# Optimization experiments

Measured on AMD Instinct MI355X. Metric: run time of the kernel, lower is better.

Reference implementation:

```python
import jax, jax.numpy as jnp
import numpy as np
import math

D_MODEL = 1024
N_HEADS = 16
FFN_DIM = 4096
B, L = 8, 1024
LN_EPS = 1e-5


def setup_inputs() -> dict:
    key = jax.random.key(0)
    ks = jax.random.split(key, 16)
    s = 1.0 / math.sqrt(D_MODEL)
    sf = 1.0 / math.sqrt(FFN_DIM)
    # weights stored [in, out] (transposed vs torch nn.Linear)
    return {
        "x": jax.random.normal(ks[0], (B, L, D_MODEL), dtype=jnp.float32),
        "Wq": jax.random.normal(ks[1], (D_MODEL, D_MODEL), dtype=jnp.float32) * s,
        "bq": jnp.zeros((D_MODEL,), jnp.float32),
        "Wk": jax.random.normal(ks[2], (D_MODEL, D_MODEL), dtype=jnp.float32) * s,
        "bk": jnp.zeros((D_MODEL,), jnp.float32),
        "Wv": jax.random.normal(ks[3], (D_MODEL, D_MODEL), dtype=jnp.float32) * s,
        "bv": jnp.zeros((D_MODEL,), jnp.float32),
        "Wo": jax.random.normal(ks[4], (D_MODEL, D_MODEL), dtype=jnp.float32) * s,
        "bo": jnp.zeros((D_MODEL,), jnp.float32),
        "W1": jax.random.normal(ks[5], (D_MODEL, FFN_DIM), dtype=jnp.float32) * s,
        "b1": jnp.zeros((FFN_DIM,), jnp.float32),
        "W2": jax.random.normal(ks[6], (FFN_DIM, D_MODEL), dtype=jnp.float32) * sf,
        "b2": jnp.zeros((D_MODEL,), jnp.float32),
        "gamma": jnp.ones((D_MODEL,), jnp.float32),
        "beta": jnp.zeros((D_MODEL,), jnp.float32),
    }


def reference(x, Wq, bq, Wk, bk, Wv, bv, Wo, bo, W1, b1, W2, b2, gamma, beta):
    Bb, Ll, D = x.shape
    H = N_HEADS
    E = D // H
    scale = 1.0 / math.sqrt(E)
    # multi-head attention (dropout is identity in eval)
    q = (x @ Wq + bq).reshape(Bb, Ll, H, E)
    k = (x @ Wk + bk).reshape(Bb, Ll, H, E)
    v = (x @ Wv + bv).reshape(Bb, Ll, H, E)
    scores = jnp.einsum('blhe,bshe->bhls', q, k)  # [B,H,L,L]
    A = jax.nn.softmax(scale * scores, axis=-1)
    ctx = jnp.einsum('bhls,bshd->blhd', A, v).reshape(Bb, Ll, D)
    attn_out = ctx @ Wo + bo
    x = x + attn_out
    # FFN: conv1d kernel_size=1 == pointwise linear; exact (erf) GELU as in F.gelu
    h = jax.nn.gelu(x @ W1 + b1, approximate=False)
    x = x + (h @ W2 + b2)
    # LayerNorm
    mu = jnp.mean(x, axis=-1, keepdims=True)
    var = jnp.mean(jnp.square(x - mu), axis=-1, keepdims=True)
    out = (x - mu) * jax.lax.rsqrt(var + LN_EPS) * gamma + beta
    return out
```

## Files before the change

kernel.cpp:

```cpp
#include <hip/hip_runtime.h>
#include <cmath>

typedef __attribute__((ext_vector_type(8))) _Float16 half8;
typedef __attribute__((ext_vector_type(4))) _Float16 half4;
typedef __attribute__((ext_vector_type(4))) float f32x4;

__device__ __forceinline__ void glds16(const void* g, void* l) {
  __builtin_amdgcn_global_load_lds(
      (__attribute__((address_space(1))) const void*)g,
      (__attribute__((address_space(3))) void*)l, 16, 0, 0);
}

__device__ __forceinline__ float fast_erf(float x) {
  float ax = fabsf(x);
  float t = 1.0f / (1.0f + 0.3275911f * ax);
  float y = t * (0.254829592f +
            t * (-0.284496736f +
            t * (1.421413741f +
            t * (-1.453152027f + t * 1.061405429f))));
  float r = 1.0f - y * __expf(-ax * ax);
  return copysignf(r, x);
}

__global__ __launch_bounds__(256) void k_cvt(const float* __restrict__ in,
                                             _Float16* __restrict__ out) {
  int i = (blockIdx.x * 256 + threadIdx.x) * 8;
  const f32x4* p = (const f32x4*)(in + i);
  f32x4 a = p[0], b = p[1];
  half8 h;
  h[0] = (_Float16)a[0]; h[1] = (_Float16)a[1]; h[2] = (_Float16)a[2]; h[3] = (_Float16)a[3];
  h[4] = (_Float16)b[0]; h[5] = (_Float16)b[1]; h[6] = (_Float16)b[2]; h[7] = (_Float16)b[3];
  *(half8*)(out + i) = h;
}

__global__ __launch_bounds__(256) void k_wt(const float* __restrict__ W,
                                            _Float16* __restrict__ Wt, int K, int N) {
  __shared__ float t[32][33];
  int x = threadIdx.x & 31, y4 = (threadIdx.x >> 5) << 2;
  int n0 = blockIdx.x << 5, k0 = blockIdx.y << 5;
#pragma unroll
  for (int r = 0; r < 4; ++r) t[y4 + r][x] = W[(size_t)(k0 + y4 + r) * N + n0 + x];
  __syncthreads();
#pragma unroll
  for (int r = 0; r < 4; ++r) Wt[(size_t)(n0 + y4 + r) * K + k0 + x] = (_Float16)t[x][y4 + r];
}

__global__ void k_biascat(const float* __restrict__ a, const float* __restrict__ b,
                          const float* __restrict__ c, float* __restrict__ o) {
  int i = blockIdx.x * 256 + threadIdx.x;
  const float* s = i < 1024 ? a : (i < 2048 ? b : c);
  o[i] = s[i & 1023];
}

template <int BM, int EPI>
__global__ __launch_bounds__(512, 2) void k_gemm8(
    const _Float16* __restrict__ A, const _Float16* __restrict__ Bt,
    const float* __restrict__ bias, const float* __restrict__ res,
    float* __restrict__ outf, _Float16* __restrict__ outh, int M, int N, int K) {
  constexpr int MR = BM / 32;
  constexpr int MH2 = MR / 2;
  constexpr int AL = BM * 64;
  constexpr int BL = 256 * 64;
  constexpr int ABYTES = BM * 128;
  constexpr int BBYTES = 256 * 128;
  constexpr int AB2 = 2 * ABYTES;
  __shared__ _Float16 lds[2 * (AL + BL)];
  const char* ldsc = (const char*)lds;

  const int tid = threadIdx.x;
  const int lane = tid & 63;
  const int w = tid >> 6, wr = w >> 2, wc = w & 3;
  const int l15 = lane & 15, grp = lane >> 4;

  const int gx = gridDim.x;
  const int nwg = gx * gridDim.y;
  const int lid = blockIdx.y * gx + blockIdx.x;
  const int wid = (lid & 7) * (nwg >> 3) + (lid >> 3);
  const int m0 = (wid / gx) * BM, n0 = (wid % gx) * 256;

  const int m2 = (l15 >> 2) & 1, m01 = l15 & 3;
  const int chunk0 = (m2 << 2) | (grp ^ m01);
  const int aoff0 = wr * 2048 + l15 * 128 + chunk0 * 16;
  const int aoff1 = aoff0 ^ 64;
  const int boff0 = wc * 2048 + l15 * 128 + chunk0 * 16;
  const int boff1 = boff0 ^ 64;

  const int srow = tid >> 3;
  const int scs8 = ((tid & 7) ^ (srow & 7)) * 8;
  const int NK = K >> 6;

  f32x4 acc[MR][4] = {};
  half8 af[MH2][2], bf[2][2];

#define STG_A(J, MHH, KN)                                                      \
  _Pragma("unroll") for (int s = 0; s < BM / 128; ++s)                         \
      glds16(A + (size_t)(m0 + (MHH) * (BM / 2) + s * 64 + srow) * K +         \
                 (size_t)(KN)*64 + scs8,                                       \
             lds + (J)*AL + ((MHH) * (BM / 2) + s * 64) * 64 + tid * 8);
#define STG_B(J, NHH, KN)                                                      \
  _Pragma("unroll") for (int s = 0; s < 2; ++s)                                \
      glds16(Bt + (size_t)(n0 + (NHH)*128 + s * 64 + srow) * K +               \
                  (size_t)(KN)*64 + scs8,                                      \
             lds + 2 * AL + (J)*BL + ((NHH)*128 + s * 64) * 64 + tid * 8);

#define VM_C asm volatile("s_waitcnt vmcnt(2)" ::: "memory")
#define VM_NONE

#define PHASE(J, MHQ, NHQ, RA, RB, STGSTMT, VMSTMT)                            \
  {                                                                            \
    if constexpr (RA) {                                                        \
      _Pragma("unroll") for (int i = 0; i < MH2; ++i) {                        \
        af[i][0] = *(const half8*)(ldsc + (J)*ABYTES +                         \
                                   ((MHQ)*MH2 + i) * 4096 + aoff0);            \
        af[i][1] = *(const half8*)(ldsc + (J)*ABYTES +                         \
                                   ((MHQ)*MH2 + i) * 4096 + aoff1);            \
      }                                                                        \
    }                                                                          \
    if constexpr (RB) {                                                        \
      _Pragma("unroll") for (int n = 0; n < 2; ++n) {                          \
        bf[n][0] = *(const half8*)(ldsc + AB2 + (J)*BBYTES +                   \
                                   ((NHQ)*2 + n) * 8192 + boff0);              \
        bf[n][1] = *(const half8*)(ldsc + AB2 + (J)*BBYTES +                   \
                                   ((NHQ)*2 + n) * 8192 + boff1);              \
      }                                                                        \
    }                                                                          \
    STGSTMT;                                                                   \
    __builtin_amdgcn_s_barrier();                                              \
    asm volatile("s_waitcnt lgkmcnt(0)");                                      \
    __builtin_amdgcn_sched_barrier(0);                                         \
    __builtin_amdgcn_s_setprio(1);                                             \
    _Pragma("unroll") for (int ks = 0; ks < 2; ++ks)                           \
        _Pragma("unroll") for (int i = 0; i < MH2; ++i)                        \
            _Pragma("unroll") for (int n = 0; n < 2; ++n)                      \
                acc[(MHQ)*MH2 + i][(NHQ)*2 + n] =                              \
                    __builtin_amdgcn_mfma_f32_16x16x32_f16(                    \
                        af[i][ks], bf[n][ks], acc[(MHQ)*MH2 + i][(NHQ)*2 + n], \
                        0, 0, 0);                                              \
    __builtin_amdgcn_s_setprio(0);                                             \
    VMSTMT;                                                                    \
    __builtin_amdgcn_s_barrier();                                              \
  }

#define KTILE(J, KT)                                                           \
  {                                                                            \
    const int kn_ = ((KT) + 1 < NK) ? (KT) + 1 : NK - 1;                       \
    const int kn2_ = ((KT) + 2 < NK) ? (KT) + 2 : NK - 1;                      \
    PHASE(J, 0, 0, true, true, STG_A(1 - (J), 0, kn_), VM_NONE)                \
    PHASE(J, 0, 1, false, true, STG_B(1 - (J), 0, kn_), VM_NONE)               \
    PHASE(J, 1, 1, true, false, STG_A(1 - (J), 1, kn_), VM_NONE)               \
    PHASE(J, 1, 0, false, true, STG_B(J, 1, kn2_), VM_C)                       \
  }

  STG_A(0, 0, 0) STG_B(0, 0, 0) STG_A(0, 1, 0) STG_B(0, 1, 0)
  STG_B(1, 1, 1)
  VM_C;
  __builtin_amdgcn_s_barrier();

#pragma unroll 1
  for (int kt = 0; kt < NK; kt += 2) {
    KTILE(0, kt)
    KTILE(1, kt + 1)
  }
  asm volatile("s_waitcnt vmcnt(0)" ::: "memory");
#undef KTILE
#undef PHASE
#undef VM_C
#undef VM_NONE
#undef STG_A
#undef STG_B

  float bcol[4];
#pragma unroll
  for (int n = 0; n < 4; ++n) bcol[n] = bias[n0 + (n * 4 + wc) * 16 + l15];
#pragma unroll
  for (int m = 0; m < MR; ++m) {
#pragma unroll
    for (int rr = 0; rr < 4; ++rr) {
      const size_t row = m0 + (m * 2 + wr) * 16 + grp * 4 + rr;
#pragma unroll
      for (int n = 0; n < 4; ++n) {
        const int col = n0 + (n * 4 + wc) * 16 + l15;
        float v = acc[m][n][rr] + bcol[n];
        const size_t idx = row * N + col;
        if (EPI == 0) {
          outh[idx] = (_Float16)v;
        } else if (EPI == 1) {
          float t2 = v + res[idx];
          outf[idx] = t2;
          outh[idx] = (_Float16)t2;
        } else if (EPI == 2) {
          float g = 0.5f * v * (1.0f + fast_erf(v * 0.70710678118654752f));
          outh[idx] = (_Float16)g;
        } else {
          outf[idx] = v + res[idx];
        }
      }
    }
  }
}

template <int EPI>
__global__ __launch_bounds__(512, 2) void k_gemmf(
    const _Float16* __restrict__ A, const _Float16* __restrict__ Bt,
    const float* __restrict__ bias, const void* __restrict__ res,
    float* __restrict__ outf, _Float16* __restrict__ outh, int M, int N, int K) {
  constexpr int AL = 256 * 64, BL = 128 * 64;
  constexpr int ABY = 32768, BBY = 16384, BBASE = 3 * ABY;
  __shared__ _Float16 lds[3 * (AL + BL)];
  const char* ldsc = (const char*)lds;

  const int tid = threadIdx.x;
  const int lane = tid & 63;
  const int w = tid >> 6, wr = w >> 1, wc = w & 1;
  const int l15 = lane & 15, grp = lane >> 4;

  const int gx = gridDim.x;
  const int nwg = gx * gridDim.y;
  const int lid = blockIdx.y * gx + blockIdx.x;
  const int wid = (lid & 7) * (nwg >> 3) + (lid >> 3);
  const int m0 = (wid / gx) * 256, n0 = (wid % gx) * 128;

  const int m2 = (l15 >> 2) & 1, m01 = l15 & 3;
  const int c0 = ((m2 << 2) | (grp ^ m01)) * 16;
  const int aoff0 = wr * 2048 + l15 * 128 + c0;
  const int aoff1 = aoff0 ^ 64;
  const int boff0 = wc * 2048 + l15 * 128 + c0;
  const int boff1 = boff0 ^ 64;

  const int srow = tid >> 3;
  const int scs8 = ((tid & 7) ^ (srow & 7)) * 8;
  const int NK = K >> 6;

  const _Float16* aG = A + (size_t)(m0 + srow) * K + scs8;
  const _Float16* bG = Bt + (size_t)(n0 + srow) * K + scs8;

  f32x4 acc[4][4] = {};

#define FSTG_A(JJ, HH, KN)                                                     \
  _Pragma("unroll") for (int s = 0; s < 2; ++s)                                \
      glds16(aG + (size_t)((HH)*128 + s * 64) * K + (size_t)(KN)*64,           \
             lds + (JJ)*AL + ((HH)*128 + s * 64) * 64 + tid * 8);
#define FSTG_B(JJ, HH, KN)                                                     \
  glds16(bG + (size_t)((HH)*64) * K + (size_t)(KN)*64,                         \
         lds + 3 * AL + (JJ)*BL + (HH)*64 * 64 + tid * 8);

#define FPHASE(PA, PB, AO, BO, STGSTMT, VMSTMT)                                \
  {                                                                            \
    half8 af_[4], bf_[4];                                                      \
    _Pragma("unroll") for (int m = 0; m < 4; ++m)                              \
        af_[m] = *(const half8*)((PA) + m * 8192 + (AO));                      \
    _Pragma("unroll") for (int n = 0; n < 4; ++n)                              \
        bf_[n] = *(const half8*)((PB) + n * 4096 + (BO));                      \
    STGSTMT;                                                                   \
    __builtin_amdgcn_s_barrier();                                              \
    asm volatile("s_waitcnt lgkmcnt(0)");                                      \
    __builtin_amdgcn_sched_barrier(0);                                         \
    __builtin_amdgcn_s_setprio(1);                                             \
    _Pragma("unroll") for (int m = 0; m < 4; ++m)                              \
        _Pragma("unroll") for (int n = 0; n < 4; ++n)                          \
            acc[m][n] = __builtin_amdgcn_mfma_f32_16x16x32_f16(                \
                af_[m], bf_[n], acc[m][n], 0, 0, 0);                           \
    __builtin_amdgcn_s_setprio(0);                                             \
    VMSTMT;                                                                    \
    __builtin_amdgcn_s_barrier();                                              \
  }

  FSTG_A(0, 0, 0) FSTG_A(0, 1, 0) FSTG_B(0, 0, 0) FSTG_B(0, 1, 0)
  FSTG_A(1, 0, 1) FSTG_A(1, 1, 1) FSTG_B(1, 0, 1) FSTG_B(1, 1, 1)
  asm volatile("s_waitcnt vmcnt(6)" ::: "memory");
  __builtin_amdgcn_s_barrier();

  int j = 0, j2 = 2;
#pragma unroll 1
  for (int kt = 0; kt < NK; ++kt) {
    const int kn = (kt + 2 < NK) ? kt + 2 : NK - 1;
    const char* pa = ldsc + j * ABY;
    const char* pb = ldsc + BBASE + j * BBY;
    FPHASE(pa, pb, aoff0, boff0, { FSTG_A(j2, 0, kn) FSTG_B(j2, 0, kn) }, )
    FPHASE(pa, pb, aoff1, boff1, { FSTG_A(j2, 1, kn) FSTG_B(j2, 1, kn) },
           asm volatile("s_waitcnt vmcnt(6)" ::: "memory");)
    j = (j == 2) ? 0 : j + 1;
    j2 = (j2 == 2) ? 0 : j2 + 1;
  }
  asm volatile("s_waitcnt vmcnt(0)" ::: "memory");
#undef FPHASE
#undef FSTG_A
#undef FSTG_B

  float bcol[4];
#pragma unroll
  for (int n = 0; n < 4; ++n) bcol[n] = bias[n0 + (n * 2 + wc) * 16 + l15];
  if (EPI == 5) {
    _Float16* vt = (_Float16*)outf;
#pragma unroll
    for (int m = 0; m < 4; ++m) {
#pragma unroll
      for (int n = 0; n < 4; ++n) {
        const int col = n0 + (n * 2 + wc) * 16 + l15;
        const size_t row0 = m0 + (m * 4 + wr) * 16 + grp * 4;
        if (col < 2048) {
#pragma unroll
          for (int rr = 0; rr < 4; ++rr)
            outh[(row0 + rr) * (size_t)N + col] = (_Float16)(acc[m][n][rr] + bcol[n]);
        } else {
          const int b = (int)(row0 >> 10), s = (int)(row0 & 1023);
          const int cv = col - 2048, hh = cv >> 6, e = cv & 63;
          half4 pk;
#pragma unroll
          for (int rr = 0; rr < 4; ++rr) pk[rr] = (_Float16)(acc[m][n][rr] + bcol[n]);
          *(half4*)&vt[((size_t)((b << 4) | hh) * 64 + e) * 1024 + s] = pk;
        }
      }
    }
    return;
  }
#pragma unroll
  for (int m = 0; m < 4; ++m) {
#pragma unroll
    for (int rr = 0; rr < 4; ++rr) {
      const size_t row = m0 + (m * 4 + wr) * 16 + grp * 4 + rr;
#pragma unroll
      for (int n = 0; n < 4; ++n) {
        const int col = n0 + (n * 2 + wc) * 16 + l15;
        float v = acc[m][n][rr] + bcol[n];
        const size_t idx = row * N + col;
        if (EPI == 0) {
          outh[idx] = (_Float16)v;
        } else if (EPI == 1) {
          float t2 = v + ((const float*)res)[idx];
          outh[idx] = (_Float16)t2;
        } else if (EPI == 2) {
          float g = 0.5f * v * (1.0f + fast_erf(v * 0.70710678118654752f));
          outh[idx] = (_Float16)g;
        } else {
          float t2 = v + (float)((const _Float16*)res)[idx];
          outf[idx] = t2;
        }
      }
    }
  }
}

__global__ __launch_bounds__(256) void k_attn(const _Float16* __restrict__ qkv,
                                              const _Float16* __restrict__ Vt,
                                              _Float16* __restrict__ ctx) {
  __shared__ _Float16 Ks[128 * 64];
  __shared__ _Float16 Vs[64 * 128];
  __shared__ _Float16 Ps[4][16 * 136];
  const int tid = threadIdx.x;
  const int lane = tid & 63, w = tid >> 6;
  const int l15 = lane & 15, grp = lane >> 4;
  const int bh = blockIdx.y, b = bh >> 4, h = bh & 15;
  const int q0 = blockIdx.x << 7;
  const float CSC = 0.125f * 1.44269504088896f;

  half8 qf[2][2];
#pragma unroll
  for (int qs = 0; qs < 2; ++qs) {
    const _Float16* qp =
        qkv + (size_t)(b * 1024 + q0 + qs * 64 + w * 16 + l15) * 3072 + h * 64 + grp * 8;
    qf[qs][0] = *(const half8*)qp;
    qf[qs][1] = *(const half8*)(qp + 32);
  }
  f32x4 octx[2][4] = {};
  float mrun[2] = {-1e30f, -1e30f}, lrun[2] = {0.f, 0.f};

  for (int kt = 0; kt < 8; ++kt) {
    const int s0 = kt * 128;
#pragma unroll
    for (int i = 0; i < 4; ++i) {
      {
        int srow = i * 32 + (tid >> 3);
        int c8 = (tid & 7) ^ (srow & 7);
        glds16(qkv + (size_t)(b * 1024 + s0 + srow) * 3072 + 1024 + h * 64 + c8 * 8,
               Ks + w * 512 + i * 2048);
      }
      {
        int erow = i * 16 + (tid >> 4);
        int c16 = (tid & 15) ^ (erow & 7);
        glds16(Vt + (size_t)(bh * 64 + erow) * 1024 + s0 + c16 * 8,
               Vs + w * 512 + i * 2048);
      }
    }
    __syncthreads();
#pragma unroll
    for (int qs = 0; qs < 2; ++qs) {
      f32x4 sacc[8] = {};
#pragma unroll
      for (int ks = 0; ks < 2; ++ks)
#pragma unroll
        for (int f = 0; f < 8; ++f) {
          int srow = f * 16 + l15;
          half8 kf = *(const half8*)&Ks[srow * 64 + ((ks * 32 + grp * 8) ^ ((srow & 7) * 8))];
          sacc[f] = __builtin_amdgcn_mfma_f32_16x16x32_f16(kf, qf[qs][ks], sacc[f], 0, 0, 0);
        }
      float sv[8][4];
      float tmax = -1e30f;
#pragma unroll
      for (int f = 0; f < 8; ++f)
#pragma unroll
        for (int r = 0; r < 4; ++r) {
          float v = sacc[f][r] * CSC;
          sv[f][r] = v;
          tmax = fmaxf(tmax, v);
        }
      tmax = fmaxf(tmax, __shfl_xor(tmax, 16));
      tmax = fmaxf(tmax, __shfl_xor(tmax, 32));
      float mnew = fmaxf(mrun[qs], tmax);
      float corr = exp2f(mrun[qs] - mnew);
      float tsum = 0.f;
#pragma unroll
      for (int f = 0; f < 8; ++f)
#pragma unroll
        for (int r = 0; r < 4; ++r) {
          float pv = exp2f(sv[f][r] - mnew);
          sv[f][r] = pv;
          tsum += pv;
        }
      tsum += __shfl_xor(tsum, 16);
      tsum += __shfl_xor(tsum, 32);
      lrun[qs] = lrun[qs] * corr + tsum;
      mrun[qs] = mnew;
#pragma unroll
      for (int r = 0; r < 4; ++r) {
        float cq = __shfl(corr, (lane & 48) + grp * 4 + r);
#pragma unroll
        for (int jf = 0; jf < 4; ++jf) octx[qs][jf][r] *= cq;
      }
#pragma unroll
      for (int f = 0; f < 8; ++f) {
        half4 pk;
        pk[0] = (_Float16)sv[f][0]; pk[1] = (_Float16)sv[f][1];
        pk[2] = (_Float16)sv[f][2]; pk[3] = (_Float16)sv[f][3];
        *(half4*)&Ps[w][l15 * 136 + f * 16 + grp * 4] = pk;
      }
#pragma unroll
      for (int ks2 = 0; ks2 < 4; ++ks2) {
        half8 pa = *(const half8*)&Ps[w][l15 * 136 + ks2 * 32 + grp * 8];
#pragma unroll
        for (int jf = 0; jf < 4; ++jf) {
          int erow = jf * 16 + l15;
          half8 vb = *(const half8*)&Vs[erow * 128 + ((ks2 * 32 + grp * 8) ^ ((erow & 7) * 8))];
          octx[qs][jf] = __builtin_amdgcn_mfma_f32_16x16x32_f16(pa, vb, octx[qs][jf], 0, 0, 0);
        }
      }
    }
    __syncthreads();
  }
#pragma unroll
  for (int qs = 0; qs < 2; ++qs) {
#pragma unroll
    for (int r = 0; r < 4; ++r) {
      float lq = __shfl(lrun[qs], (lane & 48) + grp * 4 + r);
      float inv = 1.0f / lq;
      const size_t row = b * 1024 + q0 + qs * 64 + w * 16 + grp * 4 + r;
#pragma unroll
      for (int jf = 0; jf < 4; ++jf)
        ctx[row * 1024 + h * 64 + jf * 16 + l15] = (_Float16)(octx[qs][jf][r] * inv);
    }
  }
}

__global__ __launch_bounds__(256) void k_ln(const float* xin, const float* __restrict__ gamma,
                                            const float* __restrict__ beta, float* out) {
  __shared__ float red[8];
  const int tid = threadIdx.x;
  const size_t row = blockIdx.x;
  f32x4 v = *(const f32x4*)&xin[row * 1024 + tid * 4];
  float s = v[0] + v[1] + v[2] + v[3];
  float s2 = v[0] * v[0] + v[1] * v[1] + v[2] * v[2] + v[3] * v[3];
#pragma unroll
  for (int o = 32; o >= 1; o >>= 1) {
    s += __shfl_xor(s, o);
    s2 += __shfl_xor(s2, o);
  }
  if ((tid & 63) == 0) { red[tid >> 6] = s; red[4 + (tid >> 6)] = s2; }
  __syncthreads();
  s = red[0] + red[1] + red[2] + red[3];
  s2 = red[4] + red[5] + red[6] + red[7];
  float mu = s * (1.0f / 1024.0f);
  float var = s2 * (1.0f / 1024.0f) - mu * mu;
  float rs = rsqrtf(var + 1e-5f);
  f32x4 g = *(const f32x4*)&gamma[tid * 4];
  f32x4 bt = *(const f32x4*)&beta[tid * 4];
  f32x4 o4;
#pragma unroll
  for (int r = 0; r < 4; ++r) o4[r] = (v[r] - mu) * rs * g[r] + bt[r];
  *(f32x4*)&out[row * 1024 + tid * 4] = o4;
}

extern "C" void kernel_launch(void* const* d_in, const int* in_sizes, int n_in,
                              void* d_out, int out_size, void* d_ws, size_t ws_size,
                              hipStream_t stream) {
  (void)in_sizes; (void)n_in; (void)out_size; (void)ws_size;
  const float* x  = (const float*)d_in[0];
  const float* Wq = (const float*)d_in[1];  const float* bq = (const float*)d_in[2];
  const float* Wk = (const float*)d_in[3];  const float* bk = (const float*)d_in[4];
  const float* Wv = (const float*)d_in[5];  const float* bv = (const float*)d_in[6];
  const float* Wo = (const float*)d_in[7];  const float* bo = (const float*)d_in[8];
  const float* W1 = (const float*)d_in[9];  const float* b1 = (const float*)d_in[10];
  const float* W2 = (const float*)d_in[11]; const float* b2 = (const float*)d_in[12];
  const float* gamma = (const float*)d_in[13];
  const float* beta  = (const float*)d_in[14];
  float* out = (float*)d_out;

  char* p = (char*)d_ws;
  _Float16* xb    = (_Float16*)p;  p += (size_t)16 << 20;
  _Float16* qkv   = (_Float16*)p;
  _Float16* hbuf  = (_Float16*)p;  p += (size_t)48 << 20;
  _Float16* Vt    = (_Float16*)p;  p += (size_t)16 << 20;
  _Float16* Wqkvt = (_Float16*)p;  p += (size_t)3072 * 1024 * 2;
  _Float16* Wot   = (_Float16*)p;  p += (size_t)1024 * 1024 * 2;
  _Float16* W1t   = (_Float16*)p;  p += (size_t)4096 * 1024 * 2;
  _Float16* W2t   = (_Float16*)p;  p += (size_t)4096 * 1024 * 2;
  float*    bqkv  = (float*)p;     p += (size_t)3072 * 4;
  _Float16* x1b   = (_Float16*)p;  p += (size_t)16 << 20;
  _Float16* ctx   = xb;

  k_cvt<<<4096, 256, 0, stream>>>(x, xb);
  k_wt<<<dim3(32, 32), 256, 0, stream>>>(Wq, Wqkvt, 1024, 1024);
  k_wt<<<dim3(32, 32), 256, 0, stream>>>(Wk, Wqkvt + 1024 * 1024, 1024, 1024);
  k_wt<<<dim3(32, 32), 256, 0, stream>>>(Wv, Wqkvt + 2048 * 1024, 1024, 1024);
  k_wt<<<dim3(32, 32), 256, 0, stream>>>(Wo, Wot, 1024, 1024);
  k_wt<<<dim3(128, 32), 256, 0, stream>>>(W1, W1t, 1024, 4096);
  k_wt<<<dim3(32, 128), 256, 0, stream>>>(W2, W2t, 4096, 1024);
  k_biascat<<<12, 256, 0, stream>>>(bq, bk, bv, bqkv);

  k_gemmf<5><<<dim3(24, 32), 512, 0, stream>>>(xb, Wqkvt, bqkv, nullptr, (float*)Vt, qkv,
                                               8192, 3072, 1024);
  k_attn<<<dim3(8, 128), 256, 0, stream>>>(qkv, Vt, ctx);
  k_gemmf<1><<<dim3(8, 32), 512, 0, stream>>>(ctx, Wot, bo, x, nullptr, x1b,
                                              8192, 1024, 1024);
  k_gemm8<256, 2><<<dim3(16, 32), 512, 0, stream>>>(x1b, W1t, b1, nullptr, nullptr, hbuf,
                                                    8192, 4096, 1024);
  k_gemmf<4><<<dim3(8, 32), 512, 0, stream>>>(hbuf, W2t, b2, x1b, out, nullptr,
                                              8192, 1024, 4096);
  k_ln<<<8192, 256, 0, stream>>>(out, gamma, beta, out);
}
```

Baseline: 361.0 us.

## Streamline attention softmax: fold scale into Q, lazy rescale, MFMA row sums

Folds the softmax scale and log2e factor into the Q columns in the QKV GEMM epilogue, which removes a per-score multiply in attention. Attention now skips rescaling the running max unless it grows by more than 8 (in log2 units). Row sums are computed by an extra MFMA against a ones vector instead of shuffle reductions. It also adds s_setprio around the MFMA sections and remaps the 1D grid so that consecutive blocks cover different heads and batches. Q is now stored pre-scaled in fp16, and the lazy rescale lets exp values reach up to 2^8 before they are normalised.

```diff
diff --git a/kernel.cpp b/kernel.cpp
--- a/kernel.cpp
+++ b/kernel.cpp
@@ -291,6 +291,7 @@
 #pragma unroll
   for (int n = 0; n < 4; ++n) bcol[n] = bias[n0 + (n * 2 + wc) * 16 + l15];
   if (EPI == 5) {
+    const float QSC = 0.125f * 1.44269504088896f;
     _Float16* vt = (_Float16*)outf;
 #pragma unroll
     for (int m = 0; m < 4; ++m) {
@@ -299,9 +300,10 @@
         const int col = n0 + (n * 2 + wc) * 16 + l15;
         const size_t row0 = m0 + (m * 4 + wr) * 16 + grp * 4;
         if (col < 2048) {
+          const float scl = (col < 1024) ? QSC : 1.0f;
 #pragma unroll
           for (int rr = 0; rr < 4; ++rr)
-            outh[(row0 + rr) * (size_t)N + col] = (_Float16)(acc[m][n][rr] + bcol[n]);
+            outh[(row0 + rr) * (size_t)N + col] = (_Float16)((acc[m][n][rr] + bcol[n]) * scl);
         } else {
           const int b = (int)(row0 >> 10), s = (int)(row0 & 1023);
           const int cv = col - 2048, hh = cv >> 6, e = cv & 63;
@@ -350,9 +352,10 @@
   const int tid = threadIdx.x;
   const int lane = tid & 63, w = tid >> 6;
   const int l15 = lane & 15, grp = lane >> 4;
-  const int bh = blockIdx.y, b = bh >> 4, h = bh & 15;
-  const int q0 = blockIdx.x << 7;
-  const float CSC = 0.125f * 1.44269504088896f;
+  const int d = blockIdx.x;
+  const int bh = (d & 7) * 16 + ((d >> 3) & 15);
+  const int q0 = (d >> 7) << 7;
+  const int b = bh >> 4, h = bh & 15;
 
   half8 qf[2][2];
 #pragma unroll
@@ -362,8 +365,13 @@
     qf[qs][0] = *(const half8*)qp;
     qf[qs][1] = *(const half8*)(qp + 32);
   }
+  half8 ones;
+#pragma unroll
+  for (int i = 0; i < 8; ++i) ones[i] = (_Float16)1.0f;
+
   f32x4 octx[2][4] = {};
-  float mrun[2] = {-1e30f, -1e30f}, lrun[2] = {0.f, 0.f};
+  f32x4 lsum[2] = {};
+  float mrun[2] = {-1e30f, -1e30f};
 
   for (int kt = 0; kt < 8; ++kt) {
     const int s0 = kt * 128;
@@ -386,6 +394,7 @@
 #pragma unroll
     for (int qs = 0; qs < 2; ++qs) {
       f32x4 sacc[8] = {};
+      __builtin_amdgcn_s_setprio(1);
 #pragma unroll
       for (int ks = 0; ks < 2; ++ks)
 #pragma unroll
@@ -394,49 +403,38 @@
           half8 kf = *(const half8*)&Ks[srow * 64 + ((ks * 32 + grp * 8) ^ ((srow & 7) * 8))];
           sacc[f] = __builtin_amdgcn_mfma_f32_16x16x32_f16(kf, qf[qs][ks], sacc[f], 0, 0, 0);
         }
-      float sv[8][4];
+      __builtin_amdgcn_s_setprio(0);
       float tmax = -1e30f;
 #pragma unroll
       for (int f = 0; f < 8; ++f)
 #pragma unroll
-        for (int r = 0; r < 4; ++r) {
-          float v = sacc[f][r] * CSC;
-          sv[f][r] = v;
-          tmax = fmaxf(tmax, v);
-        }
+        for (int r = 0; r < 4; ++r) tmax = fmaxf(tmax, sacc[f][r]);
       tmax = fmaxf(tmax, __shfl_xor(tmax, 16));
       tmax = fmaxf(tmax, __shfl_xor(tmax, 32));
-      float mnew = fmaxf(mrun[qs], tmax);
-      float corr = exp2f(mrun[qs] - mnew);
-      float tsum = 0.f;
-#pragma unroll
-      for (int f = 0; f < 8; ++f)
+      if (!__all(tmax <= mrun[qs] + 8.0f)) {
+        float mnew = fmaxf(mrun[qs], tmax);
+        float corr = exp2f(mrun[qs] - mnew);
+        mrun[qs] = mnew;
 #pragma unroll
         for (int r = 0; r < 4; ++r) {
-          float pv = exp2f(sv[f][r] - mnew);
-          sv[f][r] = pv;
-          tsum += pv;
+          float cq = __shfl(corr, (lane & 48) + grp * 4 + r);
+#pragma unroll
+          for (int jf = 0; jf < 4; ++jf) octx[qs][jf][r] *= cq;
+          lsum[qs][r] *= cq;
         }
-      tsum += __shfl_xor(tsum, 16);
-      tsum += __shfl_xor(tsum, 32);
-      lrun[qs] = lrun[qs] * corr + tsum;
-      mrun[qs] = mnew;
-#pragma unroll
-      for (int r = 0; r < 4; ++r) {
-        float cq = __shfl(corr, (lane & 48) + grp * 4 + r);
-#pragma unroll
-        for (int jf = 0; jf < 4; ++jf) octx[qs][jf][r] *= cq;
       }
 #pragma unroll
       for (int f = 0; f < 8; ++f) {
         half4 pk;
-        pk[0] = (_Float16)sv[f][0]; pk[1] = (_Float16)sv[f][1];
-        pk[2] = (_Float16)sv[f][2]; pk[3] = (_Float16)sv[f][3];
+#pragma unroll
+        for (int r = 0; r < 4; ++r) pk[r] = (_Float16)exp2f(sacc[f][r] - mrun[qs]);
         *(half4*)&Ps[w][l15 * 136 + f * 16 + grp * 4] = pk;
       }
+      __builtin_amdgcn_s_setprio(1);
 #pragma unroll
       for (int ks2 = 0; ks2 < 4; ++ks2) {
         half8 pa = *(const half8*)&Ps[w][l15 * 136 + ks2 * 32 + grp * 8];
+        lsum[qs] = __builtin_amdgcn_mfma_f32_16x16x32_f16(pa, ones, lsum[qs], 0, 0, 0);
 #pragma unroll
         for (int jf = 0; jf < 4; ++jf) {
           int erow = jf * 16 + l15;
@@ -444,6 +442,7 @@
           octx[qs][jf] = __builtin_amdgcn_mfma_f32_16x16x32_f16(pa, vb, octx[qs][jf], 0, 0, 0);
         }
       }
+      __builtin_amdgcn_s_setprio(0);
     }
     __syncthreads();
   }
@@ -451,8 +450,7 @@
   for (int qs = 0; qs < 2; ++qs) {
 #pragma unroll
     for (int r = 0; r < 4; ++r) {
-      float lq = __shfl(lrun[qs], (lane & 48) + grp * 4 + r);
-      float inv = 1.0f / lq;
+      float inv = 1.0f / lsum[qs][r];
       const size_t row = b * 1024 + q0 + qs * 64 + w * 16 + grp * 4 + r;
 #pragma unroll
       for (int jf = 0; jf < 4; ++jf)
@@ -528,7 +526,7 @@
 
   k_gemmf<5><<<dim3(24, 32), 512, 0, stream>>>(xb, Wqkvt, bqkv, nullptr, (float*)Vt, qkv,
                                                8192, 3072, 1024);
-  k_attn<<<dim3(8, 128), 256, 0, stream>>>(qkv, Vt, ctx);
+  k_attn<<<1024, 256, 0, stream>>>(qkv, Vt, ctx);
   k_gemmf<1><<<dim3(8, 32), 512, 0, stream>>>(ctx, Wot, bo, x, nullptr, x1b,
                                               8192, 1024, 1024);
   k_gemm8<256, 2><<<dim3(16, 32), 512, 0, stream>>>(x1b, W1t, b1, nullptr, nullptr, hbuf,
```

New measurement: 343.3 us. -4.9%, faster.
